# Performance work log

Hardware: AMD Instinct MI355X
Metric: run time of the kernel (lower is better)

Reference implementation:

```python
import jax, jax.numpy as jnp
import numpy as np

B, H, S, Dh = 8, 16, 1028, 64
G = 32
L2 = (2 * G - 1) ** 2  # 3969 relative-position entries
HID = 32
R_VAL = 4  # register-token cutoff


def setup_inputs() -> dict:
    key = jax.random.key(0)
    ks = jax.random.split(key, 7)
    return {
        "q": jax.random.normal(ks[0], (B, H, S, Dh), jnp.float32),
        "k": jax.random.normal(ks[1], (B, H, S, Dh), jnp.float32),
        "v": jax.random.normal(ks[2], (B, H, S, Dh), jnp.float32),
        # normalized log-spaced relative coords in [-1, 1], Swin-v2 style
        "rel_table": jax.random.uniform(ks[3], (L2, 2), jnp.float32, -1.0, 1.0),
        "W1": jax.random.normal(ks[4], (2, HID), jnp.float32) * 0.1,
        "b1": jnp.zeros((HID,), jnp.float32),
        "W2": jax.random.normal(ks[5], (HID, H), jnp.float32) * 0.02,
        "idx_table": jax.random.randint(ks[6], (S, S), 0, L2, jnp.int32),
        "R": R_VAL,
    }


def reference(q, k, v, rel_table, W1, b1, W2, idx_table, R):
    # CPB MLP: Linear(2->hid) + exact GELU + Linear(hid->H, no bias)
    bt = jax.nn.gelu(rel_table @ W1 + b1, approximate=False) @ W2  # [L2, H]
    # gather per-(q,kv) bias, move head axis front -> [H, S, S]
    bias = jnp.transpose(bt[idx_table], (2, 0, 1))
    pos = jnp.arange(S) >= R
    has_bias = pos[:, None] & pos[None, :]  # [S, S]
    scale = Dh ** -0.5
    scores = jnp.einsum('bhqd,bhkd->bhqk', q, k) * scale  # [B,H,S,S]
    scores = scores + jnp.where(has_bias, bias, 0.0)[None]
    p = jax.nn.softmax(scores, axis=-1)
    return jnp.einsum('bhqk,bhkd->bhqd', p, v)
```

## Files before the change

### kernel.cpp

```cpp
#include <hip/hip_runtime.h>
#include <hip/hip_bf16.h>

#define S_LEN 1028
#define DH 64
#define NHEAD 16
#define NBATCH 8
#define L2N 3969
#define HIDN 32
#define KVB 64
#define NKT 17
#define NQT 17
#define TILE_E 4096
#define LOG2E 1.4426950408889634f

typedef __bf16 bf16x8 __attribute__((ext_vector_type(8)));
typedef __bf16 bf16x4 __attribute__((ext_vector_type(4)));
typedef float f32x4 __attribute__((ext_vector_type(4)));

__device__ __forceinline__ bf16x8 cvt_bf16x8(float4 a, float4 b) {
  bf16x8 r;
  r[0] = (__bf16)a.x; r[1] = (__bf16)a.y; r[2] = (__bf16)a.z; r[3] = (__bf16)a.w;
  r[4] = (__bf16)b.x; r[5] = (__bf16)b.y; r[6] = (__bf16)b.z; r[7] = (__bf16)b.w;
  return r;
}

__device__ __forceinline__ f32x4 mfma16(bf16x8 a, bf16x8 b, f32x4 c) {
  return __builtin_amdgcn_mfma_f32_16x16x32_bf16(a, b, c, 0, 0, 0);
}

__device__ __forceinline__ float exp2_fast(float x) {
#if __has_builtin(__builtin_amdgcn_exp2f)
  return __builtin_amdgcn_exp2f(x);
#else
  return __expf(x * 0.6931471805599453f);
#endif
}

#define GLD16(gsrc, ldst)                                                     \
  __builtin_amdgcn_global_load_lds(                                           \
      (const __attribute__((address_space(1))) void*)(gsrc),                  \
      (__attribute__((address_space(3))) void*)(ldst), 16, 0, 0)

__global__ void cpb_table_lh(const float* __restrict__ rel,
                             const float* __restrict__ W1,
                             const float* __restrict__ b1,
                             const float* __restrict__ W2,
                             float* __restrict__ bt) {
  int i = blockIdx.x * blockDim.x + threadIdx.x;
  if (i >= L2N) return;
  float x = rel[2 * i], y = rel[2 * i + 1];
  float acc[NHEAD];
#pragma unroll
  for (int h = 0; h < NHEAD; ++h) acc[h] = 0.f;
#pragma unroll
  for (int j = 0; j < HIDN; ++j) {
    float t = fmaf(x, W1[j], fmaf(y, W1[HIDN + j], b1[j]));
    float g = 0.5f * t * (1.f + erff(t * 0.70710678118654752f));
#pragma unroll
    for (int h = 0; h < NHEAD; ++h) acc[h] = fmaf(g, W2[j * NHEAD + h], acc[h]);
  }
#pragma unroll
  for (int h = 0; h < NHEAD; ++h) bt[(size_t)i * NHEAD + h] = acc[h];
}

__global__ __launch_bounds__(256) void bias_expand2(const int* __restrict__ idx,
                                                    const float* __restrict__ bt,
                                                    const int* __restrict__ Rp,
                                                    __bf16* __restrict__ bias) {
  const int qrow = blockIdx.x;
  const int R = Rp[0];
  const bool qok = (qrow >= R);
  const int tid = threadIdx.x;
  __shared__ __align__(16) __bf16 strip[NHEAD][264];

  for (int k0 = 0; k0 < 1024; k0 += 256) {
    const int k = k0 + tid;
    const int l = idx[(size_t)qrow * S_LEN + k];
    const bool on = qok && (k >= R);
    const float4* btv = (const float4*)bt + (size_t)l * 4;
    float va[16];
    *(float4*)&va[0]  = btv[0];
    *(float4*)&va[4]  = btv[1];
    *(float4*)&va[8]  = btv[2];
    *(float4*)&va[12] = btv[3];
#pragma unroll
    for (int h = 0; h < NHEAD; ++h)
      strip[h][tid] = on ? (__bf16)(va[h] * LOG2E) : (__bf16)0.f;
    __syncthreads();
    {
      const int h = tid >> 4, kg = tid & 15;
      bf16x8 w0 = *(bf16x8*)&strip[h][kg * 16];
      bf16x8 w1 = *(bf16x8*)&strip[h][kg * 16 + 8];
      __bf16* dst = bias + (size_t)h * S_LEN * S_LEN + (size_t)qrow * S_LEN + k0 + kg * 16;
      *(bf16x8*)dst = w0;
      *(bf16x8*)(dst + 8) = w1;
    }
    __syncthreads();
  }
  if (tid < 64) {
    const int kt = tid & 3, h = tid >> 2;
    const int k = 1024 + kt;
    const int l = idx[(size_t)qrow * S_LEN + k];
    const bool on = qok && (k >= R);
    const float v = bt[(size_t)l * NHEAD + h];
    bias[(size_t)h * S_LEN * S_LEN + (size_t)qrow * S_LEN + k] =
        on ? (__bf16)(v * LOG2E) : (__bf16)0.f;
  }
}

__global__ __launch_bounds__(256) void kv_pack(const float* __restrict__ kg,
                                               const float* __restrict__ vg,
                                               __bf16* __restrict__ Kb,
                                               __bf16* __restrict__ Vb) {
  const int it = blockIdx.x, bh = blockIdx.y;
  const int kb = it * KVB;
  const int tid = threadIdx.x;
  const float* kp = kg + (size_t)bh * S_LEN * DH;
  const float* vp = vg + (size_t)bh * S_LEN * DH;
  __bf16* kout = Kb + ((size_t)bh * NKT + it) * TILE_E;
  __bf16* vout = Vb + ((size_t)bh * NKT + it) * TILE_E;

  for (int i = tid; i < 512; i += 256) {
    const int rho = i >> 3, gx = i & 7;
    const int e = ((rho & 15) << 2) | (rho >> 4);
    const int key = kb + e;
    const int gsrc = gx ^ (rho & 7);
    float4 a = {0.f, 0.f, 0.f, 0.f}, b = {0.f, 0.f, 0.f, 0.f};
    if (key < S_LEN) {
      a = *(const float4*)(kp + (size_t)key * DH + gsrc * 8);
      b = *(const float4*)(kp + (size_t)key * DH + gsrc * 8 + 4);
    }
    *(bf16x8*)(kout + (size_t)rho * 64 + gx * 8) = cvt_bf16x8(a, b);
  }

  __shared__ float vt[64][68];
  for (int i = tid; i < 1024; i += 256) {
    const int row = i >> 4, c4 = i & 15;
    const int key = kb + row;
    float4 a = {0.f, 0.f, 0.f, 0.f};
    if (key < S_LEN) a = *(const float4*)(vp + (size_t)key * DH + c4 * 4);
    *(float4*)&vt[row][c4 * 4] = a;
  }
  __syncthreads();
  for (int i = tid; i < 512; i += 256) {
    const int d = i >> 3, gx = i & 7;
    const int kg8 = (gx ^ (d & 7)) * 8;
    bf16x8 o;
#pragma unroll
    for (int j = 0; j < 8; ++j) o[j] = (__bf16)vt[kg8 + j][d];
    *(bf16x8*)(vout + (size_t)d * 64 + gx * 8) = o;
  }
}

#define TILE_STEP(ITC, MASKED) do {                                           \
    const int buf_ = (ITC) & 1;                                               \
    const int kk_ = (ITC) * KVB + 4 * m;                                      \
    bf16x4 bias4_[4];                                                         \
    _Pragma("unroll")                                                         \
    for (int r = 0; r < 4; ++r) {                                             \
      bf16x4 z_; z_[0] = (__bf16)0.f; z_[1] = (__bf16)0.f;                    \
      z_[2] = (__bf16)0.f; z_[3] = (__bf16)0.f;                               \
      bias4_[r] = (!(MASKED) || kk_ < S_LEN)                                  \
                      ? *(const bf16x4*)(brow[r] + kk_) : z_;                 \
    }                                                                         \
    __builtin_amdgcn_s_barrier();                                             \
    {                                                                         \
      const int nit_ = ((ITC) + 1 < NKT) ? (ITC) + 1 : 0;                     \
      const __bf16* gk_ = KbT + (size_t)nit_ * TILE_E + wave * 1024 + lo16;   \
      const __bf16* gv_ = VbT + (size_t)nit_ * TILE_E + wave * 1024 + lo16;   \
      __bf16* lk_ = &Kt[buf_ ^ 1][0][0] + wave * 1024;                        \
      __bf16* lv_ = &Vt[buf_ ^ 1][0][0] + wave * 1024;                        \
      GLD16(gk_, lk_); GLD16(gk_ + 512, lk_ + 512);                           \
      GLD16(gv_, lv_); GLD16(gv_ + 512, lv_ + 512);                           \
    }                                                                         \
    asm volatile("s_waitcnt vmcnt(8)" ::: "memory");                          \
    __builtin_amdgcn_s_barrier();                                             \
    __builtin_amdgcn_sched_barrier(0);                                        \
    f32x4 sc_[4];                                                             \
    _Pragma("unroll")                                                         \
    for (int c = 0; c < 4; ++c) {                                             \
      f32x4 a_;                                                               \
      _Pragma("unroll")                                                       \
      for (int r = 0; r < 4; ++r) a_[r] = (float)bias4_[r][c];                \
      _Pragma("unroll")                                                       \
      for (int dc = 0; dc < 2; ++dc) {                                        \
        bf16x8 kf_ = *(bf16x8*)&Kt[buf_][c * 16 + m][(dc * 32 + g * 8) ^ sw_m]; \
        a_ = mfma16(qf[dc], kf_, a_);                                         \
      }                                                                       \
      sc_[c] = a_;                                                            \
    }                                                                         \
    _Pragma("unroll")                                                         \
    for (int r = 0; r < 4; ++r) {                                             \
      float p0_ = exp2_fast(sc_[0][r]);                                       \
      float p1_ = exp2_fast(sc_[1][r]);                                       \
      float p2_ = exp2_fast(sc_[2][r]);                                       \
      float p3_ = exp2_fast(sc_[3][r]);                                       \
      if (MASKED) {                                                           \
        const float kvf_ = (kk_ < S_LEN) ? 1.f : 0.f;                         \
        lsum[r] += kvf_ * ((p0_ + p1_) + (p2_ + p3_));                        \
      } else {                                                                \
        lsum[r] += (p0_ + p1_) + (p2_ + p3_);                                 \
      }                                                                       \
      bf16x4 pb_;                                                             \
      pb_[0] = (__bf16)p0_; pb_[1] = (__bf16)p1_;                             \
      pb_[2] = (__bf16)p2_; pb_[3] = (__bf16)p3_;                             \
      const int row_ = g * 4 + r;                                             \
      *(bf16x4*)&Pl[wave][row_][(4 * m) ^ ((row_ & 7) << 3)] = pb_;           \
    }                                                                         \
    _Pragma("unroll")                                                         \
    for (int kc = 0; kc < 2; ++kc) {                                          \
      bf16x8 pf_ = *(bf16x8*)&Pl[wave][m][(kc * 32 + g * 8) ^ sw_m];          \
      _Pragma("unroll")                                                       \
      for (int t = 0; t < 4; ++t) {                                           \
        bf16x8 vf_ = *(bf16x8*)&Vt[buf_][t * 16 + m][(kc * 32 + g * 8) ^ sw_m]; \
        acc_o[t] = mfma16(pf_, vf_, acc_o[t]);                                \
      }                                                                       \
    }                                                                         \
  } while (0)

__global__ __launch_bounds__(256, 4) void flex_attn_v4(
    const float* __restrict__ qg, const __bf16* __restrict__ Kb,
    const __bf16* __restrict__ Vb, const __bf16* __restrict__ biasG,
    float* __restrict__ out) {
  const int b = blockIdx.z, h = blockIdx.y, qt = blockIdx.x;
  const int bh = b * NHEAD + h;
  const int tid = threadIdx.x;
  const int wave = tid >> 6, lane = tid & 63;
  const int g = lane >> 4, m = lane & 15;

  __shared__ __align__(16) __bf16 Kt[2][KVB][64];
  __shared__ __align__(16) __bf16 Vt[2][DH][64];
  __shared__ __align__(16) __bf16 Pl[4][16][64];

  const __bf16* KbT = Kb + (size_t)bh * NKT * TILE_E;
  const __bf16* VbT = Vb + (size_t)bh * NKT * TILE_E;
  const __bf16* bp = biasG + (size_t)h * S_LEN * S_LEN;
  const float* qp = qg + (size_t)bh * S_LEN * DH;

  const int qrow = qt * 64 + wave * 16 + m;
  const float qs = 0.125f * LOG2E;
  bf16x8 qf[2];
#pragma unroll
  for (int dc = 0; dc < 2; ++dc) {
    float4 a = {0.f, 0.f, 0.f, 0.f}, bb = {0.f, 0.f, 0.f, 0.f};
    if (qrow < S_LEN) {
      a = *(const float4*)(qp + (size_t)qrow * DH + dc * 32 + g * 8);
      bb = *(const float4*)(qp + (size_t)qrow * DH + dc * 32 + g * 8 + 4);
    }
    a.x *= qs; a.y *= qs; a.z *= qs; a.w *= qs;
    bb.x *= qs; bb.y *= qs; bb.z *= qs; bb.w *= qs;
    qf[dc] = cvt_bf16x8(a, bb);
  }

  const int qb4 = qt * 64 + wave * 16 + g * 4;
  const __bf16* brow[4];
#pragma unroll
  for (int r = 0; r < 4; ++r) {
    int qq = qb4 + r; if (qq > S_LEN - 1) qq = S_LEN - 1;
    brow[r] = bp + (size_t)qq * S_LEN;
  }

  f32x4 acc_o[4];
#pragma unroll
  for (int t = 0; t < 4; ++t) acc_o[t] = (f32x4){0.f, 0.f, 0.f, 0.f};
  float lsum[4] = {0.f, 0.f, 0.f, 0.f};

  const int sw_m = (m & 7) << 3;
  const int lo16 = lane * 8;

  {
    const __bf16* gk = KbT + wave * 1024 + lo16;
    const __bf16* gv = VbT + wave * 1024 + lo16;
    __bf16* lk = &Kt[0][0][0] + wave * 1024;
    __bf16* lv = &Vt[0][0][0] + wave * 1024;
    GLD16(gk, lk); GLD16(gk + 512, lk + 512);
    GLD16(gv, lv); GLD16(gv + 512, lv + 512);
  }

#pragma unroll 2
  for (int it = 0; it < 16; ++it) {
    TILE_STEP(it, false);
  }
  TILE_STEP(16, true);

#pragma unroll
  for (int r = 0; r < 4; ++r) {
    float s = lsum[r];
    s += __shfl_xor(s, 1);
    s += __shfl_xor(s, 2);
    s += __shfl_xor(s, 4);
    s += __shfl_xor(s, 8);
    const int qq = qb4 + r;
    if (qq >= S_LEN) continue;
    const float inv = 1.f / s;
    float* op = out + (((size_t)bh) * S_LEN + qq) * DH;
#pragma unroll
    for (int t = 0; t < 4; ++t) op[t * 16 + m] = acc_o[t][r] * inv;
  }
}

__global__ __launch_bounds__(256, 4) void flex_attn_fast(
    const float* __restrict__ qg, const float* __restrict__ kg,
    const float* __restrict__ vg, const __bf16* __restrict__ biasG,
    float* __restrict__ out) {
  const int b = blockIdx.z, h = blockIdx.y, qt = blockIdx.x;
  const int tid = threadIdx.x;
  const int wave = tid >> 6, lane = tid & 63;
  const int g = lane >> 4, m = lane & 15;

  __shared__ __align__(16) __bf16 Kt[KVB][72];
  __shared__ __align__(16) __bf16 Vt[DH][72];
  __shared__ __align__(16) __bf16 Pl[4][16][72];

  const size_t base = ((size_t)(b * NHEAD + h)) * S_LEN * DH;
  const float* qp = qg + base;
  const float* kp = kg + base;
  const float* vp = vg + base;
  const __bf16* bp = biasG + (size_t)h * S_LEN * S_LEN;

  const int qrow = qt * 64 + wave * 16 + m;
  const float qs = 0.125f * LOG2E;
  bf16x8 qf[2];
#pragma unroll
  for (int dc = 0; dc < 2; ++dc) {
    float4 a = {0.f, 0.f, 0.f, 0.f}, bb = {0.f, 0.f, 0.f, 0.f};
    if (qrow < S_LEN) {
      a = *(const float4*)(qp + (size_t)qrow * DH + dc * 32 + g * 8);
      bb = *(const float4*)(qp + (size_t)qrow * DH + dc * 32 + g * 8 + 4);
    }
    a.x *= qs; a.y *= qs; a.z *= qs; a.w *= qs;
    bb.x *= qs; bb.y *= qs; bb.z *= qs; bb.w *= qs;
    qf[dc] = cvt_bf16x8(a, bb);
  }

  f32x4 acc_o[4];
#pragma unroll
  for (int t = 0; t < 4; ++t) acc_o[t] = (f32x4){0.f, 0.f, 0.f, 0.f};
  float mrow[4], lrow[4];
#pragma unroll
  for (int r = 0; r < 4; ++r) { mrow[r] = -1e30f; lrow[r] = 0.f; }

  const int qb4 = qt * 64 + wave * 16 + g * 4;
  const int eK = wave * 16 + (lane >> 2);
  const int rowK = ((eK & 3) << 4) | (eK >> 2);
  const int colK = (lane & 3) * 16;

  for (int it = 0; it < NKT; ++it) {
    const int kb = it * KVB;
    __syncthreads();
    {
      const int krow = kb + eK;
      float4 a0 = {0,0,0,0}, a1 = {0,0,0,0}, a2 = {0,0,0,0}, a3 = {0,0,0,0};
      if (krow < S_LEN) {
        const float* src = kp + (size_t)krow * DH + colK;
        a0 = *(const float4*)(src);
        a1 = *(const float4*)(src + 4);
        a2 = *(const float4*)(src + 8);
        a3 = *(const float4*)(src + 12);
      }
      *(bf16x8*)&Kt[rowK][colK] = cvt_bf16x8(a0, a1);
      *(bf16x8*)&Kt[rowK][colK + 8] = cvt_bf16x8(a2, a3);
    }
    {
      bf16x8 p0, p1;
#pragma unroll
      for (int t = 0; t < 8; ++t) {
        const int kr = kb + wave * 16 + t;
        p0[t] = (kr < S_LEN) ? (__bf16)vp[(size_t)kr * DH + lane] : (__bf16)0.f;
      }
#pragma unroll
      for (int t = 0; t < 8; ++t) {
        const int kr = kb + wave * 16 + 8 + t;
        p1[t] = (kr < S_LEN) ? (__bf16)vp[(size_t)kr * DH + lane] : (__bf16)0.f;
      }
      *(bf16x8*)&Vt[lane][wave * 16] = p0;
      *(bf16x8*)&Vt[lane][wave * 16 + 8] = p1;
    }

    const int kk = kb + 4 * m;
    const bool kvalid = (kk < S_LEN);
    bf16x4 bias4[4];
#pragma unroll
    for (int r = 0; r < 4; ++r) {
      const int qq = (qb4 + r < S_LEN) ? qb4 + r : S_LEN - 1;
      bf16x4 z; z[0] = (__bf16)0.f; z[1] = (__bf16)0.f; z[2] = (__bf16)0.f; z[3] = (__bf16)0.f;
      bias4[r] = kvalid ? *(const bf16x4*)(bp + (size_t)qq * S_LEN + kk) : z;
    }

    __syncthreads();

    f32x4 sc[4];
#pragma unroll
    for (int c = 0; c < 4; ++c) {
      f32x4 a = (f32x4){0.f, 0.f, 0.f, 0.f};
#pragma unroll
      for (int dc = 0; dc < 2; ++dc) {
        bf16x8 kf = *(bf16x8*)&Kt[c * 16 + m][dc * 32 + g * 8];
        a = mfma16(qf[dc], kf, a);
      }
      sc[c] = a;
    }

#pragma unroll
    for (int r = 0; r < 4; ++r) {
      float s[4];
#pragma unroll
      for (int c = 0; c < 4; ++c)
        s[c] = kvalid ? sc[c][r] + (float)bias4[r][c] : -1e30f;
      float mx = fmaxf(fmaxf(s[0], s[1]), fmaxf(s[2], s[3]));
      mx = fmaxf(mx, __shfl_xor(mx, 1));
      mx = fmaxf(mx, __shfl_xor(mx, 2));
      mx = fmaxf(mx, __shfl_xor(mx, 4));
      mx = fmaxf(mx, __shfl_xor(mx, 8));
      const float mnew = fmaxf(mrow[r], mx);
      const float alpha = exp2_fast(mrow[r] - mnew);
      float p0 = exp2_fast(s[0] - mnew), p1 = exp2_fast(s[1] - mnew);
      float p2 = exp2_fast(s[2] - mnew), p3 = exp2_fast(s[3] - mnew);
      float sum = (p0 + p1) + (p2 + p3);
      sum += __shfl_xor(sum, 1);
      sum += __shfl_xor(sum, 2);
      sum += __shfl_xor(sum, 4);
      sum += __shfl_xor(sum, 8);
      lrow[r] = lrow[r] * alpha + sum;
      mrow[r] = mnew;
      bf16x4 pb;
      pb[0] = (__bf16)p0; pb[1] = (__bf16)p1; pb[2] = (__bf16)p2; pb[3] = (__bf16)p3;
      *(bf16x4*)&Pl[wave][g * 4 + r][4 * m] = pb;
#pragma unroll
      for (int t = 0; t < 4; ++t) acc_o[t][r] *= alpha;
    }

#pragma unroll
    for (int kc = 0; kc < 2; ++kc) {
      bf16x8 pf = *(bf16x8*)&Pl[wave][m][kc * 32 + g * 8];
#pragma unroll
      for (int t = 0; t < 4; ++t) {
        bf16x8 vf = *(bf16x8*)&Vt[t * 16 + m][kc * 32 + g * 8];
        acc_o[t] = mfma16(pf, vf, acc_o[t]);
      }
    }
  }

#pragma unroll
  for (int r = 0; r < 4; ++r) {
    const int qq = qb4 + r;
    if (qq >= S_LEN) continue;
    const float inv = 1.f / lrow[r];
    float* op = out + (((size_t)(b * NHEAD + h)) * S_LEN + qq) * DH;
#pragma unroll
    for (int t = 0; t < 4; ++t) op[t * 16 + m] = acc_o[t][r] * inv;
  }
}

extern "C" void kernel_launch(void* const* d_in, const int* in_sizes, int n_in,
                              void* d_out, int out_size, void* d_ws, size_t ws_size,
                              hipStream_t stream) {
  const float* q = (const float*)d_in[0];
  const float* k = (const float*)d_in[1];
  const float* v = (const float*)d_in[2];
  const float* rel = (const float*)d_in[3];
  const float* W1 = (const float*)d_in[4];
  const float* b1 = (const float*)d_in[5];
  const float* W2 = (const float*)d_in[6];
  const int* idx = (const int*)d_in[7];
  const int* Rp = (const int*)d_in[8];
  float* out = (float*)d_out;

  const size_t bt_bytes = 1u << 18;
  const size_t bias_bytes = (size_t)NHEAD * S_LEN * S_LEN * 2;
  const size_t kv_bytes = (size_t)NBATCH * NHEAD * NKT * TILE_E * 2;

  if (ws_size >= bt_bytes + bias_bytes + 2 * kv_bytes) {
    float* bt = (float*)d_ws;
    __bf16* bias = (__bf16*)((char*)d_ws + bt_bytes);
    __bf16* Kb = (__bf16*)((char*)d_ws + bt_bytes + bias_bytes);
    __bf16* Vb = (__bf16*)((char*)d_ws + bt_bytes + bias_bytes + kv_bytes);
    cpb_table_lh<<<dim3((L2N + 255) / 256), dim3(256), 0, stream>>>(rel, W1, b1, W2, bt);
    bias_expand2<<<dim3(S_LEN), dim3(256), 0, stream>>>(idx, bt, Rp, bias);
    kv_pack<<<dim3(NKT, NBATCH * NHEAD), dim3(256), 0, stream>>>(k, v, Kb, Vb);
    flex_attn_v4<<<dim3(NQT, NHEAD, NBATCH), dim3(256), 0, stream>>>(q, Kb, Vb, bias, out);
  } else {
    float* bt = (float*)d_ws;
    __bf16* bias = (__bf16*)((char*)d_ws + bt_bytes);
    cpb_table_lh<<<dim3((L2N + 255) / 256), dim3(256), 0, stream>>>(rel, W1, b1, W2, bt);
    bias_expand2<<<dim3(S_LEN), dim3(256), 0, stream>>>(idx, bt, Rp, bias);
    flex_attn_fast<<<dim3(NQT, NHEAD, NBATCH), dim3(256), 0, stream>>>(q, k, v, bias, out);
  }
}
```

Before: 276.7 us.

## Process two query tiles per block, fuse bias/KV prep, and prefetch bias

The attention kernel now handles 128 query rows per block (two 64-row sub-tiles per wave), so each staged K/V tile in LDS is reused twice and the grid shrinks to 9 query tiles. Bias values for the next KV tile are loaded into registers one step ahead with double buffering, and MFMA sections run at raised wave priority. The bias expansion and K/V packing kernels are merged into one launch whose blocks interleave both jobs. In exchange, register pressure rises (launch bounds drop to 3 waves per SIMD), and the last query tile is mostly padding.

```diff
diff --git a/kernel.cpp b/kernel.cpp
--- a/kernel.cpp
+++ b/kernel.cpp
@@ -10,6 +10,7 @@
 #define KVB 64
 #define NKT 17
 #define NQT 17
+#define NQT2 9
 #define TILE_E 4096
 #define LOG2E 1.4426950408889634f
 
@@ -63,106 +64,114 @@
   for (int h = 0; h < NHEAD; ++h) bt[(size_t)i * NHEAD + h] = acc[h];
 }
 
-__global__ __launch_bounds__(256) void bias_expand2(const int* __restrict__ idx,
-                                                    const float* __restrict__ bt,
-                                                    const int* __restrict__ Rp,
-                                                    __bf16* __restrict__ bias) {
-  const int qrow = blockIdx.x;
-  const int R = Rp[0];
-  const bool qok = (qrow >= R);
+__global__ __launch_bounds__(256) void prep_fused(
+    const int* __restrict__ idx, const float* __restrict__ bt,
+    const int* __restrict__ Rp, const float* __restrict__ kg,
+    const float* __restrict__ vg, __bf16* __restrict__ bias,
+    __bf16* __restrict__ Kb, __bf16* __restrict__ Vb) {
   const int tid = threadIdx.x;
-  __shared__ __align__(16) __bf16 strip[NHEAD][264];
-
-  for (int k0 = 0; k0 < 1024; k0 += 256) {
-    const int k = k0 + tid;
-    const int l = idx[(size_t)qrow * S_LEN + k];
-    const bool on = qok && (k >= R);
-    const float4* btv = (const float4*)bt + (size_t)l * 4;
-    float va[16];
-    *(float4*)&va[0]  = btv[0];
-    *(float4*)&va[4]  = btv[1];
-    *(float4*)&va[8]  = btv[2];
-    *(float4*)&va[12] = btv[3];
-#pragma unroll
-    for (int h = 0; h < NHEAD; ++h)
-      strip[h][tid] = on ? (__bf16)(va[h] * LOG2E) : (__bf16)0.f;
+  const int grp = blockIdx.x / 3, rem = blockIdx.x - 3 * grp;
+  __shared__ __align__(16) char smem[64 * 68 * 4];
+
+  if (rem == 0) {
+    const int qrow = grp;
+    if (qrow >= S_LEN) return;
+    __bf16(*strip)[264] = (__bf16(*)[264])smem;
+    const int R = Rp[0];
+    const bool qok = (qrow >= R);
+    for (int k0 = 0; k0 < 1024; k0 += 256) {
+      const int k = k0 + tid;
+      const int l = idx[(size_t)qrow * S_LEN + k];
+      const bool on = qok && (k >= R);
+      const float4* btv = (const float4*)bt + (size_t)l * 4;
+      float va[16];
+      *(float4*)&va[0] = btv[0];
+      *(float4*)&va[4] = btv[1];
+      *(float4*)&va[8] = btv[2];
+      *(float4*)&va[12] = btv[3];
+#pragma unroll
+      for (int h = 0; h < NHEAD; ++h)
+        strip[h][tid] = on ? (__bf16)(va[h] * LOG2E) : (__bf16)0.f;
+      __syncthreads();
+      {
+        const int h = tid >> 4, kg2 = tid & 15;
+        bf16x8 w0 = *(bf16x8*)&strip[h][kg2 * 16];
+        bf16x8 w1 = *(bf16x8*)&strip[h][kg2 * 16 + 8];
+        __bf16* dst =
+            bias + (size_t)h * S_LEN * S_LEN + (size_t)qrow * S_LEN + k0 + kg2 * 16;
+        *(bf16x8*)dst = w0;
+        *(bf16x8*)(dst + 8) = w1;
+      }
+      __syncthreads();
+    }
+    if (tid < 64) {
+      const int kt = tid & 3, h = tid >> 2;
+      const int k = 1024 + kt;
+      const int l = idx[(size_t)qrow * S_LEN + k];
+      const bool on = qok && (k >= R);
+      const float v = bt[(size_t)l * NHEAD + h];
+      bias[(size_t)h * S_LEN * S_LEN + (size_t)qrow * S_LEN + k] =
+          on ? (__bf16)(v * LOG2E) : (__bf16)0.f;
+    }
+  } else {
+    const int kvid = 2 * grp + (rem - 1);
+    if (kvid >= NKT * NBATCH * NHEAD) return;
+    const int it = kvid % NKT, bh = kvid / NKT;
+    const int kb = it * KVB;
+    const float* kp = kg + (size_t)bh * S_LEN * DH;
+    const float* vp = vg + (size_t)bh * S_LEN * DH;
+    __bf16* kout = Kb + ((size_t)bh * NKT + it) * TILE_E;
+    __bf16* vout = Vb + ((size_t)bh * NKT + it) * TILE_E;
+
+    for (int i = tid; i < 512; i += 256) {
+      const int rho = i >> 3, gx = i & 7;
+      const int e = ((rho & 15) << 2) | (rho >> 4);
+      const int key = kb + e;
+      const int gsrc = gx ^ (rho & 7);
+      float4 a = {0.f, 0.f, 0.f, 0.f}, b = {0.f, 0.f, 0.f, 0.f};
+      if (key < S_LEN) {
+        a = *(const float4*)(kp + (size_t)key * DH + gsrc * 8);
+        b = *(const float4*)(kp + (size_t)key * DH + gsrc * 8 + 4);
+      }
+      *(bf16x8*)(kout + (size_t)rho * 64 + gx * 8) = cvt_bf16x8(a, b);
+    }
+
+    float(*vt)[68] = (float(*)[68])smem;
+    for (int i = tid; i < 1024; i += 256) {
+      const int row = i >> 4, c4 = i & 15;
+      const int key = kb + row;
+      float4 a = {0.f, 0.f, 0.f, 0.f};
+      if (key < S_LEN) a = *(const float4*)(vp + (size_t)key * DH + c4 * 4);
+      *(float4*)&vt[row][c4 * 4] = a;
+    }
     __syncthreads();
-    {
-      const int h = tid >> 4, kg = tid & 15;
-      bf16x8 w0 = *(bf16x8*)&strip[h][kg * 16];
-      bf16x8 w1 = *(bf16x8*)&strip[h][kg * 16 + 8];
-      __bf16* dst = bias + (size_t)h * S_LEN * S_LEN + (size_t)qrow * S_LEN + k0 + kg * 16;
-      *(bf16x8*)dst = w0;
-      *(bf16x8*)(dst + 8) = w1;
-    }
-    __syncthreads();
-  }
-  if (tid < 64) {
-    const int kt = tid & 3, h = tid >> 2;
-    const int k = 1024 + kt;
-    const int l = idx[(size_t)qrow * S_LEN + k];
-    const bool on = qok && (k >= R);
-    const float v = bt[(size_t)l * NHEAD + h];
-    bias[(size_t)h * S_LEN * S_LEN + (size_t)qrow * S_LEN + k] =
-        on ? (__bf16)(v * LOG2E) : (__bf16)0.f;
-  }
-}
-
-__global__ __launch_bounds__(256) void kv_pack(const float* __restrict__ kg,
-                                               const float* __restrict__ vg,
-                                               __bf16* __restrict__ Kb,
-                                               __bf16* __restrict__ Vb) {
-  const int it = blockIdx.x, bh = blockIdx.y;
-  const int kb = it * KVB;
-  const int tid = threadIdx.x;
-  const float* kp = kg + (size_t)bh * S_LEN * DH;
-  const float* vp = vg + (size_t)bh * S_LEN * DH;
-  __bf16* kout = Kb + ((size_t)bh * NKT + it) * TILE_E;
-  __bf16* vout = Vb + ((size_t)bh * NKT + it) * TILE_E;
-
-  for (int i = tid; i < 512; i += 256) {
-    const int rho = i >> 3, gx = i & 7;
-    const int e = ((rho & 15) << 2) | (rho >> 4);
-    const int key = kb + e;
-    const int gsrc = gx ^ (rho & 7);
-    float4 a = {0.f, 0.f, 0.f, 0.f}, b = {0.f, 0.f, 0.f, 0.f};
-    if (key < S_LEN) {
-      a = *(const float4*)(kp + (size_t)key * DH + gsrc * 8);
-      b = *(const float4*)(kp + (size_t)key * DH + gsrc * 8 + 4);
-    }
-    *(bf16x8*)(kout + (size_t)rho * 64 + gx * 8) = cvt_bf16x8(a, b);
-  }
-
-  __shared__ float vt[64][68];
-  for (int i = tid; i < 1024; i += 256) {
-    const int row = i >> 4, c4 = i & 15;
-    const int key = kb + row;
-    float4 a = {0.f, 0.f, 0.f, 0.f};
-    if (key < S_LEN) a = *(const float4*)(vp + (size_t)key * DH + c4 * 4);
-    *(float4*)&vt[row][c4 * 4] = a;
-  }
-  __syncthreads();
-  for (int i = tid; i < 512; i += 256) {
-    const int d = i >> 3, gx = i & 7;
-    const int kg8 = (gx ^ (d & 7)) * 8;
-    bf16x8 o;
-#pragma unroll
-    for (int j = 0; j < 8; ++j) o[j] = (__bf16)vt[kg8 + j][d];
-    *(bf16x8*)(vout + (size_t)d * 64 + gx * 8) = o;
-  }
-}
-
-#define TILE_STEP(ITC, MASKED) do {                                           \
+    for (int i = tid; i < 512; i += 256) {
+      const int d = i >> 3, gx = i & 7;
+      const int kg8 = (gx ^ (d & 7)) * 8;
+      bf16x8 o;
+#pragma unroll
+      for (int j = 0; j < 8; ++j) o[j] = (__bf16)vt[kg8 + j][d];
+      *(bf16x8*)(vout + (size_t)d * 64 + gx * 8) = o;
+    }
+  }
+}
+
+#define LOADB(BB, ITC) do {                                                   \
+    const int kkL = (ITC) * KVB + 4 * m;                                      \
+    const bool okL = (kkL < S_LEN);                                           \
+    _Pragma("unroll")                                                         \
+    for (int u = 0; u < 2; ++u) {                                             \
+      _Pragma("unroll")                                                       \
+      for (int r = 0; r < 4; ++r) {                                           \
+        bf16x4 z_; z_[0] = (__bf16)0.f; z_[1] = (__bf16)0.f;                  \
+        z_[2] = (__bf16)0.f; z_[3] = (__bf16)0.f;                             \
+        BB[u][r] = okL ? *(const bf16x4*)(bp + boff[u][r] + kkL) : z_;        \
+      }                                                                       \
+    }                                                                         \
+  } while (0)
+
+#define STEP(ITC, BB, MASKED, WAITN) do {                                     \
     const int buf_ = (ITC) & 1;                                               \
-    const int kk_ = (ITC) * KVB + 4 * m;                                      \
-    bf16x4 bias4_[4];                                                         \
-    _Pragma("unroll")                                                         \
-    for (int r = 0; r < 4; ++r) {                                             \
-      bf16x4 z_; z_[0] = (__bf16)0.f; z_[1] = (__bf16)0.f;                    \
-      z_[2] = (__bf16)0.f; z_[3] = (__bf16)0.f;                               \
-      bias4_[r] = (!(MASKED) || kk_ < S_LEN)                                  \
-                      ? *(const bf16x4*)(brow[r] + kk_) : z_;                 \
-    }                                                                         \
     __builtin_amdgcn_s_barrier();                                             \
     {                                                                         \
       const int nit_ = ((ITC) + 1 < NKT) ? (ITC) + 1 : 0;                     \
@@ -173,52 +182,56 @@
       GLD16(gk_, lk_); GLD16(gk_ + 512, lk_ + 512);                           \
       GLD16(gv_, lv_); GLD16(gv_ + 512, lv_ + 512);                           \
     }                                                                         \
-    asm volatile("s_waitcnt vmcnt(8)" ::: "memory");                          \
+    asm volatile("s_waitcnt vmcnt(" #WAITN ")" ::: "memory");                 \
     __builtin_amdgcn_s_barrier();                                             \
     __builtin_amdgcn_sched_barrier(0);                                        \
-    f32x4 sc_[4];                                                             \
+    const float kvf_ = (((ITC) * KVB + 4 * m) < S_LEN) ? 1.f : 0.f;           \
     _Pragma("unroll")                                                         \
-    for (int c = 0; c < 4; ++c) {                                             \
-      f32x4 a_;                                                               \
+    for (int u = 0; u < 2; ++u) {                                             \
+      f32x4 sc_[4];                                                           \
+      __builtin_amdgcn_s_setprio(1);                                          \
       _Pragma("unroll")                                                       \
-      for (int r = 0; r < 4; ++r) a_[r] = (float)bias4_[r][c];                \
+      for (int c = 0; c < 4; ++c) {                                           \
+        f32x4 a_;                                                             \
+        _Pragma("unroll")                                                     \
+        for (int r = 0; r < 4; ++r) a_[r] = (float)BB[u][r][c];               \
+        _Pragma("unroll")                                                     \
+        for (int dc = 0; dc < 2; ++dc) {                                      \
+          bf16x8 kf_ = *(bf16x8*)&Kt[buf_][c * 16 + m][(dc * 32 + g * 8) ^ sw_m]; \
+          a_ = mfma16(qf[u][dc], kf_, a_);                                    \
+        }                                                                     \
+        sc_[c] = a_;                                                          \
+      }                                                                       \
+      __builtin_amdgcn_s_setprio(0);                                          \
       _Pragma("unroll")                                                       \
-      for (int dc = 0; dc < 2; ++dc) {                                        \
-        bf16x8 kf_ = *(bf16x8*)&Kt[buf_][c * 16 + m][(dc * 32 + g * 8) ^ sw_m]; \
-        a_ = mfma16(qf[dc], kf_, a_);                                         \
+      for (int r = 0; r < 4; ++r) {                                           \
+        float p0_ = exp2_fast(sc_[0][r]);                                     \
+        float p1_ = exp2_fast(sc_[1][r]);                                     \
+        float p2_ = exp2_fast(sc_[2][r]);                                     \
+        float p3_ = exp2_fast(sc_[3][r]);                                     \
+        if (MASKED) lsum[u][r] += kvf_ * ((p0_ + p1_) + (p2_ + p3_));         \
+        else        lsum[u][r] += (p0_ + p1_) + (p2_ + p3_);                  \
+        bf16x4 pb_;                                                           \
+        pb_[0] = (__bf16)p0_; pb_[1] = (__bf16)p1_;                           \
+        pb_[2] = (__bf16)p2_; pb_[3] = (__bf16)p3_;                           \
+        const int row_ = g * 4 + r;                                           \
+        *(bf16x4*)&Pl[wave][row_][(4 * m) ^ ((row_ & 7) << 3)] = pb_;         \
       }                                                                       \
-      sc_[c] = a_;                                                            \
-    }                                                                         \
-    _Pragma("unroll")                                                         \
-    for (int r = 0; r < 4; ++r) {                                             \
-      float p0_ = exp2_fast(sc_[0][r]);                                       \
-      float p1_ = exp2_fast(sc_[1][r]);                                       \
-      float p2_ = exp2_fast(sc_[2][r]);                                       \
-      float p3_ = exp2_fast(sc_[3][r]);                                       \
-      if (MASKED) {                                                           \
-        const float kvf_ = (kk_ < S_LEN) ? 1.f : 0.f;                         \
-        lsum[r] += kvf_ * ((p0_ + p1_) + (p2_ + p3_));                        \
-      } else {                                                                \
-        lsum[r] += (p0_ + p1_) + (p2_ + p3_);                                 \
+      __builtin_amdgcn_s_setprio(1);                                          \
+      _Pragma("unroll")                                                       \
+      for (int kc = 0; kc < 2; ++kc) {                                        \
+        bf16x8 pf_ = *(bf16x8*)&Pl[wave][m][(kc * 32 + g * 8) ^ sw_m];        \
+        _Pragma("unroll")                                                     \
+        for (int t = 0; t < 4; ++t) {                                         \
+          bf16x8 vf_ = *(bf16x8*)&Vt[buf_][t * 16 + m][(kc * 32 + g * 8) ^ sw_m]; \
+          acc_o[u][t] = mfma16(pf_, vf_, acc_o[u][t]);                        \
+        }                                                                     \
       }                                                                       \
-      bf16x4 pb_;                                                             \
-      pb_[0] = (__bf16)p0_; pb_[1] = (__bf16)p1_;                             \
-      pb_[2] = (__bf16)p2_; pb_[3] = (__bf16)p3_;                             \
-      const int row_ = g * 4 + r;                                             \
-      *(bf16x4*)&Pl[wave][row_][(4 * m) ^ ((row_ & 7) << 3)] = pb_;           \
-    }                                                                         \
-    _Pragma("unroll")                                                         \
-    for (int kc = 0; kc < 2; ++kc) {                                          \
-      bf16x8 pf_ = *(bf16x8*)&Pl[wave][m][(kc * 32 + g * 8) ^ sw_m];          \
-      _Pragma("unroll")                                                       \
-      for (int t = 0; t < 4; ++t) {                                           \
-        bf16x8 vf_ = *(bf16x8*)&Vt[buf_][t * 16 + m][(kc * 32 + g * 8) ^ sw_m]; \
-        acc_o[t] = mfma16(pf_, vf_, acc_o[t]);                                \
-      }                                                                       \
+      __builtin_amdgcn_s_setprio(0);                                          \
     }                                                                         \
   } while (0)
 
-__global__ __launch_bounds__(256, 4) void flex_attn_v4(
+__global__ __launch_bounds__(256, 3) void flex_attn_v5(
     const float* __restrict__ qg, const __bf16* __restrict__ Kb,
     const __bf16* __restrict__ Vb, const __bf16* __restrict__ biasG,
     float* __restrict__ out) {
@@ -237,37 +250,52 @@
   const __bf16* bp = biasG + (size_t)h * S_LEN * S_LEN;
   const float* qp = qg + (size_t)bh * S_LEN * DH;
 
-  const int qrow = qt * 64 + wave * 16 + m;
   const float qs = 0.125f * LOG2E;
-  bf16x8 qf[2];
-#pragma unroll
-  for (int dc = 0; dc < 2; ++dc) {
-    float4 a = {0.f, 0.f, 0.f, 0.f}, bb = {0.f, 0.f, 0.f, 0.f};
-    if (qrow < S_LEN) {
-      a = *(const float4*)(qp + (size_t)qrow * DH + dc * 32 + g * 8);
-      bb = *(const float4*)(qp + (size_t)qrow * DH + dc * 32 + g * 8 + 4);
-    }
-    a.x *= qs; a.y *= qs; a.z *= qs; a.w *= qs;
-    bb.x *= qs; bb.y *= qs; bb.z *= qs; bb.w *= qs;
-    qf[dc] = cvt_bf16x8(a, bb);
-  }
-
-  const int qb4 = qt * 64 + wave * 16 + g * 4;
-  const __bf16* brow[4];
-#pragma unroll
-  for (int r = 0; r < 4; ++r) {
-    int qq = qb4 + r; if (qq > S_LEN - 1) qq = S_LEN - 1;
-    brow[r] = bp + (size_t)qq * S_LEN;
-  }
-
-  f32x4 acc_o[4];
-#pragma unroll
-  for (int t = 0; t < 4; ++t) acc_o[t] = (f32x4){0.f, 0.f, 0.f, 0.f};
-  float lsum[4] = {0.f, 0.f, 0.f, 0.f};
+  bf16x8 qf[2][2];
+#pragma unroll
+  for (int u = 0; u < 2; ++u) {
+    const int qrow = qt * 128 + u * 64 + wave * 16 + m;
+#pragma unroll
+    for (int dc = 0; dc < 2; ++dc) {
+      float4 a = {0.f, 0.f, 0.f, 0.f}, bb = {0.f, 0.f, 0.f, 0.f};
+      if (qrow < S_LEN) {
+        a = *(const float4*)(qp + (size_t)qrow * DH + dc * 32 + g * 8);
+        bb = *(const float4*)(qp + (size_t)qrow * DH + dc * 32 + g * 8 + 4);
+      }
+      a.x *= qs; a.y *= qs; a.z *= qs; a.w *= qs;
+      bb.x *= qs; bb.y *= qs; bb.z *= qs; bb.w *= qs;
+      qf[u][dc] = cvt_bf16x8(a, bb);
+    }
+  }
+
+  int boff[2][4];
+#pragma unroll
+  for (int u = 0; u < 2; ++u)
+#pragma unroll
+    for (int r = 0; r < 4; ++r) {
+      int qq = qt * 128 + u * 64 + wave * 16 + g * 4 + r;
+      if (qq > S_LEN - 1) qq = S_LEN - 1;
+      boff[u][r] = qq * S_LEN;
+    }
+
+  f32x4 acc_o[2][4];
+#pragma unroll
+  for (int u = 0; u < 2; ++u)
+#pragma unroll
+    for (int t = 0; t < 4; ++t) acc_o[u][t] = (f32x4){0.f, 0.f, 0.f, 0.f};
+  float lsum[2][4];
+#pragma unroll
+  for (int u = 0; u < 2; ++u)
+#pragma unroll
+    for (int r = 0; r < 4; ++r) lsum[u][r] = 0.f;
 
   const int sw_m = (m & 7) << 3;
   const int lo16 = lane * 8;
 
+  bf16x4 biasA[2][4], biasB[2][4];
+
+  LOADB(biasA, 0);
+  __builtin_amdgcn_sched_barrier(0);
   {
     const __bf16* gk = KbT + wave * 1024 + lo16;
     const __bf16* gv = VbT + wave * 1024 + lo16;
@@ -277,25 +305,76 @@
     GLD16(gv, lv); GLD16(gv + 512, lv + 512);
   }
 
-#pragma unroll 2
-  for (int it = 0; it < 16; ++it) {
-    TILE_STEP(it, false);
-  }
-  TILE_STEP(16, true);
-
-#pragma unroll
-  for (int r = 0; r < 4; ++r) {
-    float s = lsum[r];
-    s += __shfl_xor(s, 1);
-    s += __shfl_xor(s, 2);
-    s += __shfl_xor(s, 4);
-    s += __shfl_xor(s, 8);
-    const int qq = qb4 + r;
-    if (qq >= S_LEN) continue;
-    const float inv = 1.f / s;
-    float* op = out + (((size_t)bh) * S_LEN + qq) * DH;
-#pragma unroll
-    for (int t = 0; t < 4; ++t) op[t * 16 + m] = acc_o[t][r] * inv;
+  for (int it = 0; it < 16; it += 2) {
+    LOADB(biasB, it + 1);
+    __builtin_amdgcn_sched_barrier(0);
+    STEP(it, biasA, false, 12);
+    LOADB(biasA, it + 2);
+    __builtin_amdgcn_sched_barrier(0);
+    STEP(it + 1, biasB, false, 12);
+  }
+  STEP(16, biasA, true, 4);
+
+#pragma unroll
+  for (int u = 0; u < 2; ++u) {
+#pragma unroll
+    for (int r = 0; r < 4; ++r) {
+      float s = lsum[u][r];
+      s += __shfl_xor(s, 1);
+      s += __shfl_xor(s, 2);
+      s += __shfl_xor(s, 4);
+      s += __shfl_xor(s, 8);
+      const int qq = qt * 128 + u * 64 + wave * 16 + g * 4 + r;
+      if (qq >= S_LEN) continue;
+      const float inv = 1.f / s;
+      float* op = out + (((size_t)bh) * S_LEN + qq) * DH;
+#pragma unroll
+      for (int t = 0; t < 4; ++t) op[t * 16 + m] = acc_o[u][t][r] * inv;
+    }
+  }
+}
+
+__global__ __launch_bounds__(256) void bias_expand2(const int* __restrict__ idx,
+                                                    const float* __restrict__ bt,
+                                                    const int* __restrict__ Rp,
+                                                    __bf16* __restrict__ bias) {
+  const int qrow = blockIdx.x;
+  const int R = Rp[0];
+  const bool qok = (qrow >= R);
+  const int tid = threadIdx.x;
+  __shared__ __align__(16) __bf16 strip[NHEAD][264];
+  for (int k0 = 0; k0 < 1024; k0 += 256) {
+    const int k = k0 + tid;
+    const int l = idx[(size_t)qrow * S_LEN + k];
+    const bool on = qok && (k >= R);
+    const float4* btv = (const float4*)bt + (size_t)l * 4;
+    float va[16];
+    *(float4*)&va[0] = btv[0];
+    *(float4*)&va[4] = btv[1];
+    *(float4*)&va[8] = btv[2];
+    *(float4*)&va[12] = btv[3];
+#pragma unroll
+    for (int h = 0; h < NHEAD; ++h)
+      strip[h][tid] = on ? (__bf16)(va[h] * LOG2E) : (__bf16)0.f;
+    __syncthreads();
+    {
+      const int h = tid >> 4, kg2 = tid & 15;
+      bf16x8 w0 = *(bf16x8*)&strip[h][kg2 * 16];
+      bf16x8 w1 = *(bf16x8*)&strip[h][kg2 * 16 + 8];
+      __bf16* dst = bias + (size_t)h * S_LEN * S_LEN + (size_t)qrow * S_LEN + k0 + kg2 * 16;
+      *(bf16x8*)dst = w0;
+      *(bf16x8*)(dst + 8) = w1;
+    }
+    __syncthreads();
+  }
+  if (tid < 64) {
+    const int kt = tid & 3, h = tid >> 2;
+    const int k = 1024 + kt;
+    const int l = idx[(size_t)qrow * S_LEN + k];
+    const bool on = qok && (k >= R);
+    const float v = bt[(size_t)l * NHEAD + h];
+    bias[(size_t)h * S_LEN * S_LEN + (size_t)qrow * S_LEN + k] =
+        on ? (__bf16)(v * LOG2E) : (__bf16)0.f;
   }
 }
 
@@ -476,9 +555,8 @@
     __bf16* Kb = (__bf16*)((char*)d_ws + bt_bytes + bias_bytes);
     __bf16* Vb = (__bf16*)((char*)d_ws + bt_bytes + bias_bytes + kv_bytes);
     cpb_table_lh<<<dim3((L2N + 255) / 256), dim3(256), 0, stream>>>(rel, W1, b1, W2, bt);
-    bias_expand2<<<dim3(S_LEN), dim3(256), 0, stream>>>(idx, bt, Rp, bias);
-    kv_pack<<<dim3(NKT, NBATCH * NHEAD), dim3(256), 0, stream>>>(k, v, Kb, Vb);
-    flex_attn_v4<<<dim3(NQT, NHEAD, NBATCH), dim3(256), 0, stream>>>(q, Kb, Vb, bias, out);
+    prep_fused<<<dim3(3264), dim3(256), 0, stream>>>(idx, bt, Rp, k, v, bias, Kb, Vb);
+    flex_attn_v5<<<dim3(NQT2, NHEAD, NBATCH), dim3(256), 0, stream>>>(q, Kb, Vb, bias, out);
   } else {
     float* bt = (float*)d_ws;
     __bf16* bias = (__bf16*)((char*)d_ws + bt_bytes);
```

New measurement: 332.6 us. +20.2%, slower.

## Fuse bias expansion with KV packing, precompute bf16 bias table, remap attention grid

Applied to the files above, without the earlier changes.

The CPB kernel now also writes a bf16 copy of the bias table pre-scaled by log2e. Bias expansion and K/V bf16 packing are merged into one kernel whose blocks are interleaved, so the gathered table reads are half the size and one launch is removed. The attention grid is remapped to put heads on the fastest axis, so blocks sharing a (batch, q-tile) run together and can share the per-head bias rows in L2. The extra bf16 table costs a small amount of workspace, and the interleaved block-role mapping adds some complexity.

```diff
diff --git a/kernel.cpp b/kernel.cpp
--- a/kernel.cpp
+++ b/kernel.cpp
@@ -12,6 +12,7 @@
 #define NQT 17
 #define TILE_E 4096
 #define LOG2E 1.4426950408889634f
+#define NKV_TILES (NKT * NBATCH * NHEAD)
 
 typedef __bf16 bf16x8 __attribute__((ext_vector_type(8)));
 typedef __bf16 bf16x4 __attribute__((ext_vector_type(4)));
@@ -45,7 +46,8 @@
                              const float* __restrict__ W1,
                              const float* __restrict__ b1,
                              const float* __restrict__ W2,
-                             float* __restrict__ bt) {
+                             float* __restrict__ bt,
+                             __bf16* __restrict__ bt16) {
   int i = blockIdx.x * blockDim.x + threadIdx.x;
   if (i >= L2N) return;
   float x = rel[2 * i], y = rel[2 * i + 1];
@@ -60,95 +62,119 @@
     for (int h = 0; h < NHEAD; ++h) acc[h] = fmaf(g, W2[j * NHEAD + h], acc[h]);
   }
 #pragma unroll
-  for (int h = 0; h < NHEAD; ++h) bt[(size_t)i * NHEAD + h] = acc[h];
-}
-
-__global__ __launch_bounds__(256) void bias_expand2(const int* __restrict__ idx,
-                                                    const float* __restrict__ bt,
-                                                    const int* __restrict__ Rp,
-                                                    __bf16* __restrict__ bias) {
-  const int qrow = blockIdx.x;
-  const int R = Rp[0];
-  const bool qok = (qrow >= R);
+  for (int h = 0; h < NHEAD; ++h) {
+    bt[(size_t)i * NHEAD + h] = acc[h];
+    bt16[(size_t)i * NHEAD + h] = (__bf16)(acc[h] * LOG2E);
+  }
+}
+
+__global__ __launch_bounds__(256) void prep_fused2(
+    const int* __restrict__ idx, const __bf16* __restrict__ bt16,
+    const int* __restrict__ Rp, const float* __restrict__ kg,
+    const float* __restrict__ vg, __bf16* __restrict__ bias,
+    __bf16* __restrict__ Kb, __bf16* __restrict__ Vb) {
   const int tid = threadIdx.x;
-  __shared__ __align__(16) __bf16 strip[NHEAD][264];
-
-  for (int k0 = 0; k0 < 1024; k0 += 256) {
-    const int k = k0 + tid;
-    const int l = idx[(size_t)qrow * S_LEN + k];
-    const bool on = qok && (k >= R);
-    const float4* btv = (const float4*)bt + (size_t)l * 4;
-    float va[16];
-    *(float4*)&va[0]  = btv[0];
-    *(float4*)&va[4]  = btv[1];
-    *(float4*)&va[8]  = btv[2];
-    *(float4*)&va[12] = btv[3];
-#pragma unroll
-    for (int h = 0; h < NHEAD; ++h)
-      strip[h][tid] = on ? (__bf16)(va[h] * LOG2E) : (__bf16)0.f;
+  const int bid = blockIdx.x;
+  __shared__ __align__(16) char smem[64 * 68 * 4];
+
+  int kvid = -1, qrow = -1;
+  if (bid < 3084) {
+    const int grp = bid / 3, rem = bid - 3 * grp;
+    if (rem == 0) qrow = grp;
+    else kvid = 2 * grp + (rem - 1);
+  } else {
+    kvid = 2056 + (bid - 3084);
+  }
+
+  if (qrow >= 0) {
+    __bf16(*strip)[520] = (__bf16(*)[520])smem;
+    const int R = Rp[0];
+    const bool qok = (qrow >= R);
+    const __bf16* bsrc = bt16;
+    bf16x8 z8;
+#pragma unroll
+    for (int j = 0; j < 8; ++j) z8[j] = (__bf16)0.f;
+
+    for (int k0 = 0; k0 < 1024; k0 += 512) {
+      const int ka = k0 + tid, kb2 = k0 + 256 + tid;
+      const int la = idx[(size_t)qrow * S_LEN + ka];
+      const int lb = idx[(size_t)qrow * S_LEN + kb2];
+      bf16x8 va0 = *(const bf16x8*)(bsrc + (size_t)la * 16);
+      bf16x8 va1 = *(const bf16x8*)(bsrc + (size_t)la * 16 + 8);
+      bf16x8 vb0 = *(const bf16x8*)(bsrc + (size_t)lb * 16);
+      bf16x8 vb1 = *(const bf16x8*)(bsrc + (size_t)lb * 16 + 8);
+      const bool ona = qok && (ka >= R);
+      const bool onb = qok && (kb2 >= R);
+      if (!ona) { va0 = z8; va1 = z8; }
+      if (!onb) { vb0 = z8; vb1 = z8; }
+#pragma unroll
+      for (int h = 0; h < 8; ++h) {
+        strip[h][tid] = va0[h];
+        strip[h][256 + tid] = vb0[h];
+        strip[8 + h][tid] = va1[h];
+        strip[8 + h][256 + tid] = vb1[h];
+      }
+      __syncthreads();
+      {
+        const int h = tid >> 4, seg = tid & 15;
+        __bf16* dst = bias + (size_t)h * S_LEN * S_LEN + (size_t)qrow * S_LEN +
+                      k0 + seg * 32;
+#pragma unroll
+        for (int j = 0; j < 4; ++j) {
+          bf16x8 w = *(bf16x8*)&strip[h][seg * 32 + j * 8];
+          *(bf16x4*)(dst + j * 8) = *(bf16x4*)&w;
+          *(bf16x4*)(dst + j * 8 + 4) = *((bf16x4*)&w + 1);
+        }
+      }
+      __syncthreads();
+    }
+    if (tid < 64) {
+      const int kt = tid & 3, h = tid >> 2;
+      const int k = 1024 + kt;
+      const int l = idx[(size_t)qrow * S_LEN + k];
+      const bool on = qok && (k >= R);
+      bias[(size_t)h * S_LEN * S_LEN + (size_t)qrow * S_LEN + k] =
+          on ? bt16[(size_t)l * 16 + h] : (__bf16)0.f;
+    }
+  } else {
+    if (kvid >= NKV_TILES) return;
+    const int it = kvid % NKT, bh = kvid / NKT;
+    const int kb = it * KVB;
+    const float* kp = kg + (size_t)bh * S_LEN * DH;
+    const float* vp = vg + (size_t)bh * S_LEN * DH;
+    __bf16* kout = Kb + ((size_t)bh * NKT + it) * TILE_E;
+    __bf16* vout = Vb + ((size_t)bh * NKT + it) * TILE_E;
+
+    for (int i = tid; i < 512; i += 256) {
+      const int rho = i >> 3, gx = i & 7;
+      const int e = ((rho & 15) << 2) | (rho >> 4);
+      const int key = kb + e;
+      const int gsrc = gx ^ (rho & 7);
+      float4 a = {0.f, 0.f, 0.f, 0.f}, b = {0.f, 0.f, 0.f, 0.f};
+      if (key < S_LEN) {
+        a = *(const float4*)(kp + (size_t)key * DH + gsrc * 8);
+        b = *(const float4*)(kp + (size_t)key * DH + gsrc * 8 + 4);
+      }
+      *(bf16x8*)(kout + (size_t)rho * 64 + gx * 8) = cvt_bf16x8(a, b);
+    }
+
+    float(*vt)[68] = (float(*)[68])smem;
+    for (int i = tid; i < 1024; i += 256) {
+      const int row = i >> 4, c4 = i & 15;
+      const int key = kb + row;
+      float4 a = {0.f, 0.f, 0.f, 0.f};
+      if (key < S_LEN) a = *(const float4*)(vp + (size_t)key * DH + c4 * 4);
+      *(float4*)&vt[row][c4 * 4] = a;
+    }
     __syncthreads();
-    {
-      const int h = tid >> 4, kg = tid & 15;
-      bf16x8 w0 = *(bf16x8*)&strip[h][kg * 16];
-      bf16x8 w1 = *(bf16x8*)&strip[h][kg * 16 + 8];
-      __bf16* dst = bias + (size_t)h * S_LEN * S_LEN + (size_t)qrow * S_LEN + k0 + kg * 16;
-      *(bf16x8*)dst = w0;
-      *(bf16x8*)(dst + 8) = w1;
-    }
-    __syncthreads();
-  }
-  if (tid < 64) {
-    const int kt = tid & 3, h = tid >> 2;
-    const int k = 1024 + kt;
-    const int l = idx[(size_t)qrow * S_LEN + k];
-    const bool on = qok && (k >= R);
-    const float v = bt[(size_t)l * NHEAD + h];
-    bias[(size_t)h * S_LEN * S_LEN + (size_t)qrow * S_LEN + k] =
-        on ? (__bf16)(v * LOG2E) : (__bf16)0.f;
-  }
-}
-
-__global__ __launch_bounds__(256) void kv_pack(const float* __restrict__ kg,
-                                               const float* __restrict__ vg,
-                                               __bf16* __restrict__ Kb,
-                                               __bf16* __restrict__ Vb) {
-  const int it = blockIdx.x, bh = blockIdx.y;
-  const int kb = it * KVB;
-  const int tid = threadIdx.x;
-  const float* kp = kg + (size_t)bh * S_LEN * DH;
-  const float* vp = vg + (size_t)bh * S_LEN * DH;
-  __bf16* kout = Kb + ((size_t)bh * NKT + it) * TILE_E;
-  __bf16* vout = Vb + ((size_t)bh * NKT + it) * TILE_E;
-
-  for (int i = tid; i < 512; i += 256) {
-    const int rho = i >> 3, gx = i & 7;
-    const int e = ((rho & 15) << 2) | (rho >> 4);
-    const int key = kb + e;
-    const int gsrc = gx ^ (rho & 7);
-    float4 a = {0.f, 0.f, 0.f, 0.f}, b = {0.f, 0.f, 0.f, 0.f};
-    if (key < S_LEN) {
-      a = *(const float4*)(kp + (size_t)key * DH + gsrc * 8);
-      b = *(const float4*)(kp + (size_t)key * DH + gsrc * 8 + 4);
-    }
-    *(bf16x8*)(kout + (size_t)rho * 64 + gx * 8) = cvt_bf16x8(a, b);
-  }
-
-  __shared__ float vt[64][68];
-  for (int i = tid; i < 1024; i += 256) {
-    const int row = i >> 4, c4 = i & 15;
-    const int key = kb + row;
-    float4 a = {0.f, 0.f, 0.f, 0.f};
-    if (key < S_LEN) a = *(const float4*)(vp + (size_t)key * DH + c4 * 4);
-    *(float4*)&vt[row][c4 * 4] = a;
-  }
-  __syncthreads();
-  for (int i = tid; i < 512; i += 256) {
-    const int d = i >> 3, gx = i & 7;
-    const int kg8 = (gx ^ (d & 7)) * 8;
-    bf16x8 o;
-#pragma unroll
-    for (int j = 0; j < 8; ++j) o[j] = (__bf16)vt[kg8 + j][d];
-    *(bf16x8*)(vout + (size_t)d * 64 + gx * 8) = o;
+    for (int i = tid; i < 512; i += 256) {
+      const int d = i >> 3, gx = i & 7;
+      const int kg8 = (gx ^ (d & 7)) * 8;
+      bf16x8 o;
+#pragma unroll
+      for (int j = 0; j < 8; ++j) o[j] = (__bf16)vt[kg8 + j][d];
+      *(bf16x8*)(vout + (size_t)d * 64 + gx * 8) = o;
+    }
   }
 }
 
@@ -218,11 +244,14 @@
     }                                                                         \
   } while (0)
 
-__global__ __launch_bounds__(256, 4) void flex_attn_v4(
+__global__ __launch_bounds__(256, 4) void flex_attn_v4x(
     const float* __restrict__ qg, const __bf16* __restrict__ Kb,
     const __bf16* __restrict__ Vb, const __bf16* __restrict__ biasG,
     float* __restrict__ out) {
-  const int b = blockIdx.z, h = blockIdx.y, qt = blockIdx.x;
+  const int h = blockIdx.x;
+  const int y = blockIdx.y;
+  const int qt = y % NQT;
+  const int b = y / NQT;
   const int bh = b * NHEAD + h;
   const int tid = threadIdx.x;
   const int wave = tid >> 6, lane = tid & 63;
@@ -296,6 +325,50 @@
     float* op = out + (((size_t)bh) * S_LEN + qq) * DH;
 #pragma unroll
     for (int t = 0; t < 4; ++t) op[t * 16 + m] = acc_o[t][r] * inv;
+  }
+}
+
+__global__ __launch_bounds__(256) void bias_expand2(const int* __restrict__ idx,
+                                                    const float* __restrict__ bt,
+                                                    const int* __restrict__ Rp,
+                                                    __bf16* __restrict__ bias) {
+  const int qrow = blockIdx.x;
+  const int R = Rp[0];
+  const bool qok = (qrow >= R);
+  const int tid = threadIdx.x;
+  __shared__ __align__(16) __bf16 strip[NHEAD][264];
+  for (int k0 = 0; k0 < 1024; k0 += 256) {
+    const int k = k0 + tid;
+    const int l = idx[(size_t)qrow * S_LEN + k];
+    const bool on = qok && (k >= R);
+    const float4* btv = (const float4*)bt + (size_t)l * 4;
+    float va[16];
+    *(float4*)&va[0] = btv[0];
+    *(float4*)&va[4] = btv[1];
+    *(float4*)&va[8] = btv[2];
+    *(float4*)&va[12] = btv[3];
+#pragma unroll
+    for (int h = 0; h < NHEAD; ++h)
+      strip[h][tid] = on ? (__bf16)(va[h] * LOG2E) : (__bf16)0.f;
+    __syncthreads();
+    {
+      const int h = tid >> 4, kg2 = tid & 15;
+      bf16x8 w0 = *(bf16x8*)&strip[h][kg2 * 16];
+      bf16x8 w1 = *(bf16x8*)&strip[h][kg2 * 16 + 8];
+      __bf16* dst = bias + (size_t)h * S_LEN * S_LEN + (size_t)qrow * S_LEN + k0 + kg2 * 16;
+      *(bf16x8*)dst = w0;
+      *(bf16x8*)(dst + 8) = w1;
+    }
+    __syncthreads();
+  }
+  if (tid < 64) {
+    const int kt = tid & 3, h = tid >> 2;
+    const int k = 1024 + kt;
+    const int l = idx[(size_t)qrow * S_LEN + k];
+    const bool on = qok && (k >= R);
+    const float v = bt[(size_t)l * NHEAD + h];
+    bias[(size_t)h * S_LEN * S_LEN + (size_t)qrow * S_LEN + k] =
+        on ? (__bf16)(v * LOG2E) : (__bf16)0.f;
   }
 }
 
@@ -467,23 +540,24 @@
   float* out = (float*)d_out;
 
   const size_t bt_bytes = 1u << 18;
+  const size_t bt16_bytes = 1u << 17;
   const size_t bias_bytes = (size_t)NHEAD * S_LEN * S_LEN * 2;
   const size_t kv_bytes = (size_t)NBATCH * NHEAD * NKT * TILE_E * 2;
 
-  if (ws_size >= bt_bytes + bias_bytes + 2 * kv_bytes) {
-    float* bt = (float*)d_ws;
-    __bf16* bias = (__bf16*)((char*)d_ws + bt_bytes);
-    __bf16* Kb = (__bf16*)((char*)d_ws + bt_bytes + bias_bytes);
-    __bf16* Vb = (__bf16*)((char*)d_ws + bt_bytes + bias_bytes + kv_bytes);
-    cpb_table_lh<<<dim3((L2N + 255) / 256), dim3(256), 0, stream>>>(rel, W1, b1, W2, bt);
-    bias_expand2<<<dim3(S_LEN), dim3(256), 0, stream>>>(idx, bt, Rp, bias);
-    kv_pack<<<dim3(NKT, NBATCH * NHEAD), dim3(256), 0, stream>>>(k, v, Kb, Vb);
-    flex_attn_v4<<<dim3(NQT, NHEAD, NBATCH), dim3(256), 0, stream>>>(q, Kb, Vb, bias, out);
+  float* bt = (float*)d_ws;
+  __bf16* bt16 = (__bf16*)((char*)d_ws + bt_bytes);
+  __bf16* bias = (__bf16*)((char*)d_ws + bt_bytes + bt16_bytes);
+  __bf16* Kb = (__bf16*)((char*)d_ws + bt_bytes + bt16_bytes + bias_bytes);
+  __bf16* Vb = (__bf16*)((char*)d_ws + bt_bytes + bt16_bytes + bias_bytes + kv_bytes);
+
+  if (ws_size >= bt_bytes + bt16_bytes + bias_bytes + 2 * kv_bytes) {
+    cpb_table_lh<<<dim3((L2N + 255) / 256), dim3(256), 0, stream>>>(rel, W1, b1, W2, bt, bt16);
+    prep_fused2<<<dim3(3204), dim3(256), 0, stream>>>(idx, bt16, Rp, k, v, bias, Kb, Vb);
+    flex_attn_v4x<<<dim3(NHEAD, NQT * NBATCH, 1), dim3(256), 0, stream>>>(q, Kb, Vb, bias, out);
   } else {
-    float* bt = (float*)d_ws;
-    __bf16* bias = (__bf16*)((char*)d_ws + bt_bytes);
-    cpb_table_lh<<<dim3((L2N + 255) / 256), dim3(256), 0, stream>>>(rel, W1, b1, W2, bt);
-    bias_expand2<<<dim3(S_LEN), dim3(256), 0, stream>>>(idx, bt, Rp, bias);
-    flex_attn_fast<<<dim3(NQT, NHEAD, NBATCH), dim3(256), 0, stream>>>(q, k, v, bias, out);
-  }
-}
+    __bf16* bias_f = (__bf16*)((char*)d_ws + bt_bytes + bt16_bytes);
+    cpb_table_lh<<<dim3((L2N + 255) / 256), dim3(256), 0, stream>>>(rel, W1, b1, W2, bt, bt16);
+    bias_expand2<<<dim3(S_LEN), dim3(256), 0, stream>>>(idx, bt, Rp, bias_f);
+    flex_attn_fast<<<dim3(NQT, NHEAD, NBATCH), dim3(256), 0, stream>>>(q, k, v, bias_f, out);
+  }
+}
```

New measurement: 252.7 us. 1.1x faster.
